# Optimization experiments

Measured on AMD Instinct MI355X. Metric: run time of the kernel, lower is better.

## Reference

```python
import jax, jax.numpy as jnp
import numpy as np

B = 64
D_MODEL = 2048
D_SSM = 4096      # expand * d_model
HEADDIM = 64
NHEADS = 64       # D_SSM // HEADDIM
D_STATE = 128
D_IN_PROJ = 2 * D_SSM + 2 * D_STATE + NHEADS  # 8512, d_mlp == 0
ACT_LEVELS = 2 ** (8 - 1) - 1  # 127
W_LEVELS = 2 ** (8 - 1) - 1


def fake_quant(x, levels):
    # symmetric absmax fake-quant along last dim with straight-through estimator
    scale = jnp.max(jnp.abs(x), axis=-1, keepdims=True) / levels
    scale = jnp.where(scale == 0, 1.0, scale)
    q = jnp.round(x / scale) * scale
    return x + jax.lax.stop_gradient(q - x)


def quant_linear(x, W):
    # QuantLinear: fake-quant activations (per row) and weights (per output channel)
    xq = fake_quant(x, ACT_LEVELS)
    Wq = fake_quant(W, W_LEVELS)
    return xq @ Wq.T


def softplus_taylor3(x):
    return jnp.log(2.0) + 0.5 * x + x ** 2 / 8.0 + x ** 3 / 48.0


def exp_taylor5(x):
    return 1.0 + x + x ** 2 / 2.0 + x ** 3 / 6.0 + x ** 4 / 24.0 + x ** 5 / 120.0


def setup_inputs() -> dict:
    key = jax.random.key(0)
    k = jax.random.split(key, 7)
    hidden_states = jax.random.normal(k[0], (B, 1, D_MODEL), dtype=jnp.float32)
    ssm_state = jax.random.normal(k[1], (B, NHEADS, HEADDIM, D_STATE), dtype=jnp.float32) * 0.1
    W_in = jax.random.normal(k[2], (D_IN_PROJ, D_MODEL), dtype=jnp.float32) * (1.0 / np.sqrt(D_MODEL))
    # dt_bias = inverse-softplus of dt ~ LogUniform(1e-3, 1e-1)
    dt = jnp.exp(jax.random.uniform(k[3], (NHEADS,)) * (np.log(0.1) - np.log(0.001)) + np.log(0.001))
    dt_bias = dt + jnp.log(-jnp.expm1(-dt))
    A_log = jnp.log(jax.random.uniform(k[4], (NHEADS,), minval=1.0, maxval=16.0))
    Dp = jnp.ones((D_SSM,), dtype=jnp.float32)
    W_out = jax.random.normal(k[5], (D_MODEL, D_SSM), dtype=jnp.float32) * (1.0 / np.sqrt(D_SSM))
    return {"hidden_states": hidden_states, "ssm_state": ssm_state, "W_in": W_in,
            "dt_bias": dt_bias, "A_log": A_log, "D": Dp, "W_out": W_out}


def reference(hidden_states, ssm_state, W_in, dt_bias, A_log, D, W_out):
    dtype = hidden_states.dtype
    b = hidden_states.shape[0]
    zxbcdt = quant_linear(hidden_states[:, 0, :], W_in)  # [b, 8512]
    z = zxbcdt[:, :D_SSM]
    xBC = zxbcdt[:, D_SSM:2 * D_SSM + 2 * D_STATE]
    dt = zxbcdt[:, -NHEADS:]
    # activation fake-quant on xBC (STE)
    xBC = fake_quant(xBC, ACT_LEVELS)
    x = xBC[:, :D_SSM]                                   # [b, d_ssm]
    Bm = xBC[:, D_SSM:D_SSM + D_STATE]                   # [b, n]
    C = xBC[:, D_SSM + D_STATE:]                         # [b, n]
    A = -jnp.exp(A_log.astype(jnp.float32))              # [h]
    # no_sftplus: piecewise 3rd-order Taylor softplus
    dt = dt + dt_bias.astype(dt.dtype)
    dt = jnp.where(dt < -2.0, 0.0, jnp.where(dt > 2.0, dt, softplus_taylor3(dt)))
    # taylor_exp: clipped 5th-order Taylor exp of dt*A
    dA = jnp.maximum(dt * A, -10000.0)
    scale = jnp.clip(exp_taylor5(dA), 0.0, 1.0)          # [b, h]
    xh = x.reshape(b, NHEADS, HEADDIM)                   # [b, h, p]
    dBx = jnp.einsum('bh,bn,bhp->bhpn', dt, Bm, xh)
    ssm_state = ssm_state * scale[:, :, None, None] + dBx  # [b, h, p, n]
    y = jnp.einsum('bhpn,bn->bhp', ssm_state.astype(dtype), C).reshape(b, D_SSM)
    y = fake_quant(y, ACT_LEVELS)
    y = y + D.astype(dtype) * x                          # per-channel skip (D has d_ssm entries)
    y = y * jax.nn.relu(z)
    y = fake_quant(y, ACT_LEVELS)
    out = quant_linear(y, W_out)                         # [b, d_model]
    return out[:, None, :]
```

## Files before the change

### kernel.cpp

```cpp
#include <hip/hip_runtime.h>


#define B_       64
#define DMODEL   2048
#define DSSM     4096
#define NH       64
#define HD       64
#define DSTATE   128
#define DPROJ    8512
#define XBCLEN   4352

typedef __attribute__((ext_vector_type(4))) int int4v;
typedef __attribute__((ext_vector_type(4))) float f4v;

__device__ __forceinline__ float blockMax256(float v, float* sm) {
  #pragma unroll
  for (int off = 32; off > 0; off >>= 1)
    v = fmaxf(v, __shfl_xor(v, off, 64));
  __syncthreads();
  if ((threadIdx.x & 63) == 0) sm[threadIdx.x >> 6] = v;
  __syncthreads();
  return fmaxf(fmaxf(sm[0], sm[1]), fmaxf(sm[2], sm[3]));
}

__device__ __forceinline__ float absmax4(float4 v) {
  return fmaxf(fmaxf(fabsf(v.x), fabsf(v.y)), fmaxf(fabsf(v.z), fabsf(v.w)));
}

__device__ __forceinline__ float absmax4v(f4v v) {
  return fmaxf(fmaxf(fabsf(v.x), fabsf(v.y)), fmaxf(fabsf(v.z), fabsf(v.w)));
}

__device__ __forceinline__ float waveMax(float v) {
  #pragma unroll
  for (int off = 32; off > 0; off >>= 1)
    v = fmaxf(v, __shfl_xor(v, off, 64));
  return v;
}

__device__ __forceinline__ unsigned int pack4(float a, float b, float c, float d,
                                              float rs) {
  int c0 = (int)rintf(a * rs), c1 = (int)rintf(b * rs);
  int c2 = (int)rintf(c * rs), c3 = (int)rintf(d * rs);
  return (unsigned)(c0 & 255) | ((unsigned)(c1 & 255) << 8) |
         ((unsigned)(c2 & 255) << 16) | ((unsigned)(c3 & 255) << 24);
}

__global__ __launch_bounds__(256) void quantx(const float* __restrict__ in,
                                              unsigned int* __restrict__ outq,
                                              float* __restrict__ scales) {
  __shared__ float sm[4];
  int r = blockIdx.x;
  const float4* row = (const float4*)(in + (size_t)r * DMODEL);
  float4 v[2];
  float m = 0.f;
  #pragma unroll
  for (int i = 0; i < 2; i++) {
    v[i] = row[threadIdx.x + i * 256];
    m = fmaxf(m, absmax4(v[i]));
  }
  float mx = blockMax256(m, sm);
  float s = mx * (1.0f / 127.0f);
  float rs = (s == 0.f) ? 0.f : 127.0f / mx;
  if (s == 0.f) s = 1.f;
  if (threadIdx.x == 0) scales[r] = s;
  unsigned int* orow = outq + (size_t)r * (DMODEL / 4);
  #pragma unroll
  for (int i = 0; i < 2; i++)
    orow[threadIdx.x + i * 256] = pack4(v[i].x, v[i].y, v[i].z, v[i].w, rs);
}

template<int K, int ROWS>
__global__ __launch_bounds__(256) void fgemm(const float* __restrict__ W,
                                             const char* __restrict__ Aq,
                                             const float* __restrict__ sA,
                                             float* __restrict__ Cout, int N) {
  constexpr int NF4 = K / 256;
  constexpr int RPW = ROWS / 4;
  constexpr int LSTRIDE = K / 4 + 4;
  __shared__ unsigned int wq[ROWS * LSTRIDE];
  __shared__ float smax[ROWS];
  int t = threadIdx.x, wave = t >> 6, lane = t & 63;
  int n0 = blockIdx.x * ROWS;
  #pragma unroll
  for (int rr = 0; rr < RPW; rr++) {
    int row = wave * RPW + rr;
    const f4v* rp = (const f4v*)(W + (size_t)(n0 + row) * K);
    f4v v[NF4];
    float m = 0.f;
    #pragma unroll
    for (int c = 0; c < NF4; c++) {
      v[c] = __builtin_nontemporal_load(&rp[lane + c * 64]);
      m = fmaxf(m, absmax4v(v[c]));
    }
    m = waveMax(m);
    float s = (m == 0.f) ? 1.f : m * (1.0f / 127.0f);
    float rs = (m == 0.f) ? 0.f : 127.0f / m;
    if (lane == 0) smax[row] = s;
    unsigned int* wrow = wq + row * LSTRIDE;
    #pragma unroll
    for (int c = 0; c < NF4; c++)
      wrow[lane + c * 64] = pack4(v[c].x, v[c].y, v[c].z, v[c].w, rs);
  }
  __syncthreads();
  int l16 = lane & 15, quad = lane >> 4;
  int4v acc = {0, 0, 0, 0};
  const char* arow = Aq + (size_t)(wave * 16 + l16) * K + quad * 16;
  const unsigned int* brow = wq + l16 * LSTRIDE + quad * 4;
  for (int k = 0; k < K; k += 256) {
    int4v af[4], bf[4];
    #pragma unroll
    for (int u = 0; u < 4; u++)
      af[u] = *(const int4v*)(arow + k + u * 64);
    #pragma unroll
    for (int u = 0; u < 4; u++) {
      int4v z = {0, 0, 0, 0};
      bf[u] = z;
      if (l16 < ROWS) bf[u] = *(const int4v*)(brow + (k + u * 64) / 4);
    }
    #pragma unroll
    for (int u = 0; u < 4; u++)
      acc = __builtin_amdgcn_mfma_i32_16x16x64_i8(af[u], bf[u], acc, 0, 0, 0);
  }
  if (l16 < ROWS) {
    float sw = smax[l16];
    #pragma unroll
    for (int r = 0; r < 4; r++) {
      int m = wave * 16 + quad * 4 + r;
      Cout[(size_t)m * N + n0 + l16] = (float)acc[r] * sA[m] * sw;
    }
  }
}

__global__ __launch_bounds__(256) void kyf(const float* __restrict__ state,
                                           const float* __restrict__ zxb,
                                           const float* __restrict__ dt_bias,
                                           const float* __restrict__ A_log,
                                           float* __restrict__ yraw) {
  __shared__ float sm[4];
  int hx = blockIdx.x, b = blockIdx.y, t = threadIdx.x;
  int lane = t & 63;
  const float* prow = zxb + (size_t)b * DPROJ;
  const float4* p4 = (const float4*)prow;
  float m = 0.f;
  #pragma unroll
  for (int i = 0; i < 5; i++) {
    int idx = 1024 + t + i * 256;
    if (idx < 2112) m = fmaxf(m, absmax4(p4[idx]));
  }
  float mx = blockMax256(m, sm);
  float s = mx * (1.0f / 127.0f);
  float rs = (s == 0.f) ? 0.f : 127.0f / mx;
  if (s == 0.f) s = 1.f;
  float4 craw = p4[2080 + (t & 31)];
  float4 c4;
  c4.x = rintf(craw.x * rs) * s;
  c4.y = rintf(craw.y * rs) * s;
  c4.z = rintf(craw.z * rs) * s;
  c4.w = rintf(craw.w * rs) * s;
  float p = 0.f;
  if (lane < 32) {
    float4 braw = p4[2048 + lane];
    float4 bq;
    bq.x = rintf(braw.x * rs) * s;
    bq.y = rintf(braw.y * rs) * s;
    bq.z = rintf(braw.z * rs) * s;
    bq.w = rintf(braw.w * rs) * s;
    p = bq.x * c4.x + bq.y * c4.y + bq.z * c4.z + bq.w * c4.w;
  }
  #pragma unroll
  for (int off = 1; off < 32; off <<= 1) p += __shfl_xor(p, off, 64);
  float sbc = __shfl(p, 0, 64);
  #pragma unroll
  for (int hh = 0; hh < 2; hh++) {
    int h = hx * 2 + hh;
    float dtv = prow[2 * DSSM + 2 * DSTATE + h] + dt_bias[h];
    if (dtv < -2.f) dtv = 0.f;
    else if (dtv <= 2.f)
      dtv = 0.6931471805599453f + 0.5f * dtv + dtv * dtv * (1.f / 8.f)
            + dtv * dtv * dtv * (1.f / 48.f);
    float A = -expf(A_log[h]);
    float dA = fmaxf(dtv * A, -10000.f);
    float e = 1.f + dA + dA * dA * (1.f / 2.f) + dA * dA * dA * (1.f / 6.f)
              + dA * dA * dA * dA * (1.f / 24.f)
              + dA * dA * dA * dA * dA * (1.f / 120.f);
    e = fminf(fmaxf(e, 0.f), 1.f);
    float coef = dtv * sbc;
    const f4v* st = (const f4v*)(state + ((size_t)b * NH + h) * (HD * DSTATE));
    f4v s4[8];
    #pragma unroll
    for (int j = 0; j < 8; j++) s4[j] = __builtin_nontemporal_load(&st[j * 256 + t]);
    float acc[8];
    #pragma unroll
    for (int j = 0; j < 8; j++)
      acc[j] = s4[j].x * c4.x + s4[j].y * c4.y + s4[j].z * c4.z + s4[j].w * c4.w;
    #pragma unroll
    for (int off = 1; off < 32; off <<= 1) {
      #pragma unroll
      for (int j = 0; j < 8; j++) acc[j] += __shfl_xor(acc[j], off, 64);
    }
    if ((t & 31) == 0) {
      #pragma unroll
      for (int j = 0; j < 8; j++) {
        int r = j * 8 + (t >> 5);
        int d = h * HD + r;
        float xr = prow[DSSM + d];
        float xq = rintf(xr * rs) * s;
        yraw[(size_t)b * DSSM + d] = e * acc[j] + coef * xq;
      }
    }
  }
}

__global__ __launch_bounds__(256) void kepif(const float* __restrict__ yraw,
                                             const float* __restrict__ zxb,
                                             const float* __restrict__ Dv,
                                             unsigned int* __restrict__ q3,
                                             float* __restrict__ sy) {
  __shared__ float sm[4];
  int b = blockIdx.x, t = threadIdx.x;
  const float4* p4 = (const float4*)(zxb + (size_t)b * DPROJ);
  float mq = 0.f;
  #pragma unroll
  for (int i = 0; i < 5; i++) {
    int idx = 1024 + t + i * 256;
    if (idx < 2112) mq = fmaxf(mq, absmax4(p4[idx]));
  }
  float mxq = blockMax256(mq, sm);
  float sq = mxq * (1.0f / 127.0f);
  float rsq = (sq == 0.f) ? 0.f : 127.0f / mxq;
  if (sq == 0.f) sq = 1.f;
  const float* yrow = yraw + (size_t)b * DSSM;
  float4 yv[4];
  float m = 0.f;
  #pragma unroll
  for (int i = 0; i < 4; i++) {
    yv[i] = *(const float4*)(yrow + t * 4 + i * 1024);
    m = fmaxf(m, absmax4(yv[i]));
  }
  float mx1 = blockMax256(m, sm);
  float s1 = mx1 * (1.0f / 127.0f);
  float rs1 = (s1 == 0.f) ? 0.f : 127.0f / mx1;
  if (s1 == 0.f) s1 = 1.f;
  float4 y3[4];
  float m2 = 0.f;
  #pragma unroll
  for (int i = 0; i < 4; i++) {
    int fi = t + i * 256;
    float4 xr = p4[1024 + fi];
    float4 x4;
    x4.x = rintf(xr.x * rsq) * sq;
    x4.y = rintf(xr.y * rsq) * sq;
    x4.z = rintf(xr.z * rsq) * sq;
    x4.w = rintf(xr.w * rsq) * sq;
    float4 z4 = p4[fi];
    float4 d4 = ((const float4*)Dv)[fi];
    float4 r;
    r.x = (rintf(yv[i].x * rs1) * s1 + d4.x * x4.x) * fmaxf(z4.x, 0.f);
    r.y = (rintf(yv[i].y * rs1) * s1 + d4.y * x4.y) * fmaxf(z4.y, 0.f);
    r.z = (rintf(yv[i].z * rs1) * s1 + d4.z * x4.z) * fmaxf(z4.z, 0.f);
    r.w = (rintf(yv[i].w * rs1) * s1 + d4.w * x4.w) * fmaxf(z4.w, 0.f);
    y3[i] = r;
    m2 = fmaxf(m2, absmax4(r));
  }
  float mx3 = blockMax256(m2, sm);
  float s3 = mx3 * (1.0f / 127.0f);
  float rs3 = (s3 == 0.f) ? 0.f : 127.0f / mx3;
  if (s3 == 0.f) s3 = 1.f;
  if (t == 0) sy[b] = s3;
  unsigned int* orow = q3 + (size_t)b * (DSSM / 4);
  #pragma unroll
  for (int i = 0; i < 4; i++)
    orow[t + i * 256] = pack4(y3[i].x, y3[i].y, y3[i].z, y3[i].w, rs3);
}

extern "C" void kernel_launch(void* const* d_in, const int* in_sizes, int n_in,
                              void* d_out, int out_size, void* d_ws, size_t ws_size,
                              hipStream_t stream) {
  const float* hidden  = (const float*)d_in[0];
  const float* ssm     = (const float*)d_in[1];
  const float* W_in    = (const float*)d_in[2];
  const float* dt_bias = (const float*)d_in[3];
  const float* A_log   = (const float*)d_in[4];
  const float* Dv      = (const float*)d_in[5];
  const float* W_out   = (const float*)d_in[6];
  float* out = (float*)d_out;

  char* p = (char*)d_ws;
  auto alloc = [&](size_t bytes) {
    char* r = p;
    p += (bytes + 255) & ~(size_t)255;
    return r;
  };
  unsigned int* xq = (unsigned int*)alloc((size_t)B_ * DMODEL);
  unsigned int* q3 = (unsigned int*)alloc((size_t)B_ * DSSM);
  float* sx    = (float*)alloc(B_ * 4);
  float* sy    = (float*)alloc(B_ * 4);
  float* zxb   = (float*)alloc((size_t)B_ * DPROJ * 4);
  float* yraw  = (float*)alloc((size_t)B_ * DSSM * 4);

  quantx<<<B_, 256, 0, stream>>>(hidden, xq, sx);
  fgemm<DMODEL, 16><<<DPROJ / 16, 256, 0, stream>>>(W_in, (const char*)xq, sx,
                                                    zxb, DPROJ);
  kyf<<<dim3(NH / 2, B_), 256, 0, stream>>>(ssm, zxb, dt_bias, A_log, yraw);
  kepif<<<B_, 256, 0, stream>>>(yraw, zxb, Dv, q3, sy);
  fgemm<DSSM, 4><<<DMODEL / 4, 256, 0, stream>>>(W_out, (const char*)q3, sy,
                                                 out, DMODEL);
}
```

Baseline: 285.1 us.

## Fuse SSM scan and epilogue kernels via atomic last-block-per-row completion

Merges the per-head SSM output kernel with the per-row epilogue quantization kernel. Each block atomically max-reduces its output absmax into a per-batch slot and increments a counter, and the last block for each batch row performs the quantize, skip, gate and requantize epilogue. It also issues the first head's state loads before the absmax reduction so they overlap it. This removes one kernel launch and a redundant absmax pass over yraw. In exchange it adds atomics, fences and a serialized tail where a single block per row does the epilogue.

Measured after the change: 684.3 us. 2.4x slower.

```diff
diff --git a/kernel.cpp b/kernel.cpp
--- a/kernel.cpp
+++ b/kernel.cpp
@@ -48,7 +48,9 @@
 
 __global__ __launch_bounds__(256) void quantx(const float* __restrict__ in,
                                               unsigned int* __restrict__ outq,
-                                              float* __restrict__ scales) {
+                                              float* __restrict__ scales,
+                                              unsigned* __restrict__ ymax_u,
+                                              unsigned* __restrict__ cnt) {
   __shared__ float sm[4];
   int r = blockIdx.x;
   const float4* row = (const float4*)(in + (size_t)r * DMODEL);
@@ -63,7 +65,11 @@
   float s = mx * (1.0f / 127.0f);
   float rs = (s == 0.f) ? 0.f : 127.0f / mx;
   if (s == 0.f) s = 1.f;
-  if (threadIdx.x == 0) scales[r] = s;
+  if (threadIdx.x == 0) {
+    scales[r] = s;
+    ymax_u[r] = 0u;
+    cnt[r] = 0u;
+  }
   unsigned int* orow = outq + (size_t)r * (DMODEL / 4);
   #pragma unroll
   for (int i = 0; i < 2; i++)
@@ -132,16 +138,27 @@
   }
 }
 
-__global__ __launch_bounds__(256) void kyf(const float* __restrict__ state,
-                                           const float* __restrict__ zxb,
-                                           const float* __restrict__ dt_bias,
-                                           const float* __restrict__ A_log,
-                                           float* __restrict__ yraw) {
+__global__ __launch_bounds__(256) void kysef(const float* __restrict__ state,
+                                             const float* __restrict__ zxb,
+                                             const float* __restrict__ dt_bias,
+                                             const float* __restrict__ A_log,
+                                             const float* __restrict__ Dv,
+                                             float* __restrict__ yraw,
+                                             unsigned int* __restrict__ q3,
+                                             float* __restrict__ sy,
+                                             unsigned* __restrict__ ymax_u,
+                                             unsigned* __restrict__ cnt) {
   __shared__ float sm[4];
+  __shared__ unsigned oldS;
   int hx = blockIdx.x, b = blockIdx.y, t = threadIdx.x;
   int lane = t & 63;
   const float* prow = zxb + (size_t)b * DPROJ;
   const float4* p4 = (const float4*)prow;
+  int h0 = hx * 2;
+  const f4v* st0 = (const f4v*)(state + ((size_t)b * NH + h0) * (HD * DSTATE));
+  f4v s4[8];
+  #pragma unroll
+  for (int j = 0; j < 8; j++) s4[j] = __builtin_nontemporal_load(&st0[j * 256 + t]);
   float m = 0.f;
   #pragma unroll
   for (int i = 0; i < 5; i++) {
@@ -171,9 +188,16 @@
   #pragma unroll
   for (int off = 1; off < 32; off <<= 1) p += __shfl_xor(p, off, 64);
   float sbc = __shfl(p, 0, 64);
+  float ymy = 0.f;
   #pragma unroll
   for (int hh = 0; hh < 2; hh++) {
-    int h = hx * 2 + hh;
+    int h = h0 + hh;
+    if (hh == 1) {
+      const f4v* st1 = (const f4v*)(state + ((size_t)b * NH + h) * (HD * DSTATE));
+      #pragma unroll
+      for (int j = 0; j < 8; j++)
+        s4[j] = __builtin_nontemporal_load(&st1[j * 256 + t]);
+    }
     float dtv = prow[2 * DSSM + 2 * DSTATE + h] + dt_bias[h];
     if (dtv < -2.f) dtv = 0.f;
     else if (dtv <= 2.f)
@@ -186,10 +210,6 @@
               + dA * dA * dA * dA * dA * (1.f / 120.f);
     e = fminf(fmaxf(e, 0.f), 1.f);
     float coef = dtv * sbc;
-    const f4v* st = (const f4v*)(state + ((size_t)b * NH + h) * (HD * DSTATE));
-    f4v s4[8];
-    #pragma unroll
-    for (int j = 0; j < 8; j++) s4[j] = __builtin_nontemporal_load(&st[j * 256 + t]);
     float acc[8];
     #pragma unroll
     for (int j = 0; j < 8; j++)
@@ -206,60 +226,50 @@
         int d = h * HD + r;
         float xr = prow[DSSM + d];
         float xq = rintf(xr * rs) * s;
-        yraw[(size_t)b * DSSM + d] = e * acc[j] + coef * xq;
+        float yv = e * acc[j] + coef * xq;
+        yraw[(size_t)b * DSSM + d] = yv;
+        ymy = fmaxf(ymy, fabsf(yv));
       }
     }
   }
-}
-
-__global__ __launch_bounds__(256) void kepif(const float* __restrict__ yraw,
-                                             const float* __restrict__ zxb,
-                                             const float* __restrict__ Dv,
-                                             unsigned int* __restrict__ q3,
-                                             float* __restrict__ sy) {
-  __shared__ float sm[4];
-  int b = blockIdx.x, t = threadIdx.x;
-  const float4* p4 = (const float4*)(zxb + (size_t)b * DPROJ);
-  float mq = 0.f;
-  #pragma unroll
-  for (int i = 0; i < 5; i++) {
-    int idx = 1024 + t + i * 256;
-    if (idx < 2112) mq = fmaxf(mq, absmax4(p4[idx]));
-  }
-  float mxq = blockMax256(mq, sm);
-  float sq = mxq * (1.0f / 127.0f);
-  float rsq = (sq == 0.f) ? 0.f : 127.0f / mxq;
-  if (sq == 0.f) sq = 1.f;
-  const float* yrow = yraw + (size_t)b * DSSM;
-  float4 yv[4];
-  float m = 0.f;
-  #pragma unroll
-  for (int i = 0; i < 4; i++) {
-    yv[i] = *(const float4*)(yrow + t * 4 + i * 1024);
-    m = fmaxf(m, absmax4(yv[i]));
-  }
-  float mx1 = blockMax256(m, sm);
+  float mblk = blockMax256(ymy, sm);
+  if (t == 0)
+    __hip_atomic_fetch_max(&ymax_u[b], __float_as_uint(mblk),
+                           __ATOMIC_RELAXED, __HIP_MEMORY_SCOPE_AGENT);
+  __threadfence();
+  unsigned old = 0;
+  if (t == 0)
+    old = __hip_atomic_fetch_add(&cnt[b], 1u, __ATOMIC_ACQ_REL,
+                                 __HIP_MEMORY_SCOPE_AGENT);
+  if (t == 0) oldS = old;
+  __syncthreads();
+  if (oldS != (NH / 2 - 1)) return;
+  __threadfence();
+  float mx1 = __uint_as_float(
+      __hip_atomic_load(&ymax_u[b], __ATOMIC_RELAXED, __HIP_MEMORY_SCOPE_AGENT));
   float s1 = mx1 * (1.0f / 127.0f);
   float rs1 = (s1 == 0.f) ? 0.f : 127.0f / mx1;
   if (s1 == 0.f) s1 = 1.f;
+  const float* yrow = yraw + (size_t)b * DSSM;
   float4 y3[4];
   float m2 = 0.f;
   #pragma unroll
   for (int i = 0; i < 4; i++) {
     int fi = t + i * 256;
+    float4 yv4 = *(const float4*)(yrow + fi * 4);
     float4 xr = p4[1024 + fi];
     float4 x4;
-    x4.x = rintf(xr.x * rsq) * sq;
-    x4.y = rintf(xr.y * rsq) * sq;
-    x4.z = rintf(xr.z * rsq) * sq;
-    x4.w = rintf(xr.w * rsq) * sq;
+    x4.x = rintf(xr.x * rs) * s;
+    x4.y = rintf(xr.y * rs) * s;
+    x4.z = rintf(xr.z * rs) * s;
+    x4.w = rintf(xr.w * rs) * s;
     float4 z4 = p4[fi];
     float4 d4 = ((const float4*)Dv)[fi];
     float4 r;
-    r.x = (rintf(yv[i].x * rs1) * s1 + d4.x * x4.x) * fmaxf(z4.x, 0.f);
-    r.y = (rintf(yv[i].y * rs1) * s1 + d4.y * x4.y) * fmaxf(z4.y, 0.f);
-    r.z = (rintf(yv[i].z * rs1) * s1 + d4.z * x4.z) * fmaxf(z4.z, 0.f);
-    r.w = (rintf(yv[i].w * rs1) * s1 + d4.w * x4.w) * fmaxf(z4.w, 0.f);
+    r.x = (rintf(yv4.x * rs1) * s1 + d4.x * x4.x) * fmaxf(z4.x, 0.f);
+    r.y = (rintf(yv4.y * rs1) * s1 + d4.y * x4.y) * fmaxf(z4.y, 0.f);
+    r.z = (rintf(yv4.z * rs1) * s1 + d4.z * x4.z) * fmaxf(z4.z, 0.f);
+    r.w = (rintf(yv4.w * rs1) * s1 + d4.w * x4.w) * fmaxf(z4.w, 0.f);
     y3[i] = r;
     m2 = fmaxf(m2, absmax4(r));
   }
@@ -298,12 +308,14 @@
   float* sy    = (float*)alloc(B_ * 4);
   float* zxb   = (float*)alloc((size_t)B_ * DPROJ * 4);
   float* yraw  = (float*)alloc((size_t)B_ * DSSM * 4);
-
-  quantx<<<B_, 256, 0, stream>>>(hidden, xq, sx);
+  unsigned* ymax_u = (unsigned*)alloc(B_ * 4);
+  unsigned* cnt    = (unsigned*)alloc(B_ * 4);
+
+  quantx<<<B_, 256, 0, stream>>>(hidden, xq, sx, ymax_u, cnt);
   fgemm<DMODEL, 16><<<DPROJ / 16, 256, 0, stream>>>(W_in, (const char*)xq, sx,
                                                     zxb, DPROJ);
-  kyf<<<dim3(NH / 2, B_), 256, 0, stream>>>(ssm, zxb, dt_bias, A_log, yraw);
-  kepif<<<B_, 256, 0, stream>>>(yraw, zxb, Dv, q3, sy);
+  kysef<<<dim3(NH / 2, B_), 256, 0, stream>>>(ssm, zxb, dt_bias, A_log, Dv,
+                                              yraw, q3, sy, ymax_u, cnt);
   fgemm<DSSM, 4><<<DMODEL / 4, 256, 0, stream>>>(W_out, (const char*)q3, sy,
                                                  out, DMODEL);
 }
```
